# Kernel optimization log

Measured on AMD Instinct MI355X. Metric: run time of the kernel, lower is better.

The kernel has to match this reference:

```python
import jax, jax.numpy as jnp
import numpy as np

N = 20000
E = 320000
H = 4
IN_DIM = 2000
# (in_dim, per-head out channels, concat) for each GATConv layer
LAYER_DIMS = [(2000, 128, True), (512, 64, True), (256, 32, True), (128, 64, False)]
NEG_SLOPE = 0.2  # PyG GATConv LeakyReLU slope


def setup_inputs() -> dict:
    key = jax.random.key(0)
    ks = jax.random.split(key, 2 + 4 * len(LAYER_DIMS))
    inp = {
        "x": jax.random.normal(ks[0], (N, IN_DIM), dtype=jnp.float32),
        "edge_index": jax.random.randint(ks[1], (2, E), 0, N, dtype=jnp.int64),
    }
    for i, (din, c, concat) in enumerate(LAYER_DIMS):
        k0, k1, k2, _ = jax.random.split(ks[2 + i], 4)
        inp[f"W{i}"] = (jax.random.normal(k0, (din, H * c), dtype=jnp.float32)
                         * (1.0 / np.sqrt(din)).astype(np.float32))
        inp[f"as{i}"] = jax.random.normal(k1, (H, c), dtype=jnp.float32) * 0.1
        inp[f"ad{i}"] = jax.random.normal(k2, (H, c), dtype=jnp.float32) * 0.1
        inp[f"b{i}"] = jnp.zeros((H * c if concat else c,), dtype=jnp.float32)
    return inp


def gat_conv(x, src, dst, W, att_src, att_dst, bias, concat):
    n, c = x.shape[0], W.shape[1] // H
    h = (x @ W).reshape(n, H, c)                      # (N,H,C) per-head features
    a_s = jnp.einsum("nhc,hc->nh", h, att_src)        # (N,H) source logits
    a_d = jnp.einsum("nhc,hc->nh", h, att_dst)        # (N,H) target logits
    e = a_s[src] + a_d[dst]                           # (E,H) per-edge logits
    e = jnp.where(e > 0, e, NEG_SLOPE * e)            # leaky_relu
    # segment softmax over edges sharing the same target node
    m = jax.ops.segment_max(e, dst, num_segments=n)   # (N,H)
    ex = jnp.exp(e - m[dst])
    denom = jax.ops.segment_sum(ex, dst, num_segments=n)
    alpha = ex / denom[dst]                           # (E,H)
    # weighted scatter-aggregate of source features
    out = jax.ops.segment_sum(alpha[:, :, None] * h[src], dst, num_segments=n)  # (N,H,C)
    out = out.reshape(n, H * c) if concat else out.mean(axis=1)
    return out + bias


def reference(x, edge_index, W0, as0, ad0, b0, W1, as1, ad1, b1,
              W2, as2, ad2, b2, W3, as3, ad3, b3):
    loops = jnp.arange(N, dtype=edge_index.dtype)
    src = jnp.concatenate([edge_index[0], loops])     # add self-loops (PyG default)
    dst = jnp.concatenate([edge_index[1], loops])
    params = [(W0, as0, ad0, b0), (W1, as1, ad1, b1), (W2, as2, ad2, b2), (W3, as3, ad3, b3)]
    h = x
    for i, (W, a_s, a_d, b) in enumerate(params):
        concat = LAYER_DIMS[i][2]
        h = gat_conv(h, src, dst, W, a_s, a_d, b, concat)
        if i < len(params) - 1:
            h = jax.nn.elu(h)  # dropout inactive in eval mode
    return h
```

## Files before the change

kernel.cpp:

```cpp
#include <hip/hip_runtime.h>
#include <hip/hip_bf16.h>

#define GN 20000
#define GE 320000
#define GETOT (GE + GN)
#define GH 4
#define NROW 20096

typedef __attribute__((ext_vector_type(8))) _Float16 f16x8;
typedef __attribute__((ext_vector_type(4))) float f32x4;

__global__ void detect_dtype_kernel(const void* __restrict__ ei, int* __restrict__ flag) {
    if (threadIdx.x == 0 && blockIdx.x == 0) {
        const long long* p = (const long long*)ei;
        int ok = 1;
        for (int i = 0; i < 16; ++i) {
            long long v = p[i];
            if (v < 0 || v >= GN) ok = 0;
        }
        *flag = ok;
    }
}

__device__ __forceinline__ int load_idx(const void* ei, int is64, long long pos) {
    if (is64) return (int)((const long long*)ei)[pos];
    return ((const int*)ei)[pos];
}

__global__ void hist_kernel(const void* __restrict__ ei, const int* __restrict__ flagp,
                            int* __restrict__ counts) {
    int e = blockIdx.x * blockDim.x + threadIdx.x;
    if (e >= GETOT) return;
    int d;
    if (e < GE) d = load_idx(ei, *flagp, (long long)GE + e);
    else        d = e - GE;
    atomicAdd(&counts[d], 1);
}

__global__ void scan_kernel(const int* __restrict__ counts, int* __restrict__ offsets,
                            int* __restrict__ cursor) {
    __shared__ int sh[1024];
    int tid = threadIdx.x;
    int carry = 0;
    for (int base = 0; base < GN; base += 1024) {
        int i = base + tid;
        int v = (i < GN) ? counts[i] : 0;
        sh[tid] = v;
        __syncthreads();
        for (int o = 1; o < 1024; o <<= 1) {
            int t = (tid >= o) ? sh[tid - o] : 0;
            __syncthreads();
            sh[tid] += t;
            __syncthreads();
        }
        int excl = carry + sh[tid] - v;
        if (i < GN) { offsets[i] = excl; cursor[i] = excl; }
        carry += sh[1023];
        __syncthreads();
    }
    if (tid == 0) offsets[GN] = carry;
}

__global__ void scatter_kernel(const void* __restrict__ ei, const int* __restrict__ flagp,
                               int* __restrict__ cursor, int* __restrict__ csr_src) {
    int e = blockIdx.x * blockDim.x + threadIdx.x;
    if (e >= GETOT) return;
    int s, d;
    if (e < GE) {
        int is64 = *flagp;
        s = load_idx(ei, is64, e);
        d = load_idx(ei, is64, (long long)GE + e);
    } else {
        s = d = e - GE;
    }
    int pos = atomicAdd(&cursor[d], 1);
    csr_src[pos] = s;
}

__device__ __forceinline__ float h2f(unsigned u) {
    unsigned short us = (unsigned short)u;
    _Float16 h;
    __builtin_memcpy(&h, &us, 2);
    return (float)h;
}
__device__ __forceinline__ unsigned short f2h_bits(float v) {
    _Float16 h = (_Float16)v;
    unsigned short us;
    __builtin_memcpy(&us, &h, 2);
    return us;
}

__global__ __launch_bounds__(256) void convert_xf16(const float* __restrict__ x,
                                                    unsigned* __restrict__ xf) {
    const int CPR = 2016 / 8;
    long long idx = (long long)blockIdx.x * 256 + threadIdx.x;
    if (idx >= (long long)NROW * CPR) return;
    int row = (int)(idx / CPR);
    int col = (int)(idx % CPR) * 8;
    uint4 hp = make_uint4(0, 0, 0, 0);
    if (row < GN && col < 2000) {
        const float* p = x + (size_t)row * 2000 + col;
        float4 v0 = *(const float4*)p, v1 = *(const float4*)(p + 4);
        hp.x = (unsigned)f2h_bits(v0.x) | ((unsigned)f2h_bits(v0.y) << 16);
        hp.y = (unsigned)f2h_bits(v0.z) | ((unsigned)f2h_bits(v0.w) << 16);
        hp.z = (unsigned)f2h_bits(v1.x) | ((unsigned)f2h_bits(v1.y) << 16);
        hp.w = (unsigned)f2h_bits(v1.z) | ((unsigned)f2h_bits(v1.w) << 16);
    }
    *(uint4*)(xf + (((size_t)row * 2016 + col) >> 1)) = hp;
}

__global__ void convert_wt(const float* __restrict__ W,
                           _Float16* __restrict__ thi,
                           int K, int N, int Kpad) {
    __shared__ float tile[32][33];
    int kb = blockIdx.x * 32, nb = blockIdx.y * 32;
    for (int i = threadIdx.y; i < 32; i += 8) {
        int k = kb + i, n = nb + threadIdx.x;
        tile[i][threadIdx.x] = (k < K) ? W[(size_t)k * N + n] : 0.f;
    }
    __syncthreads();
    for (int i = threadIdx.y; i < 32; i += 8) {
        int n = nb + i, k = kb + threadIdx.x;
        thi[(size_t)n * Kpad + k] = (_Float16)tile[threadIdx.x][i];
    }
}

__device__ __forceinline__ int swz(int a) { return a ^ (((a >> 6) & 7) << 4); }
__device__ __forceinline__ int invswz(int p) {
    int b8 = (p >> 8) & 1, b7 = (p >> 7) & 1;
    int a6 = ((p >> 6) & 1) ^ b8;
    int a5 = ((p >> 5) & 1) ^ b7;
    int a4 = ((p >> 4) & 1) ^ a6;
    return (p & ~0x70) | (a4 << 4) | (a5 << 5) | (a6 << 6);
}

#define GLDS16(gsrc, ldst) __builtin_amdgcn_global_load_lds( \
    (const __attribute__((address_space(1))) void*)(gsrc),   \
    (__attribute__((address_space(3))) void*)(ldst), 16, 0, 0)

template <int MODE>
__global__ __launch_bounds__(256, 4) void gemm_f16(
        const _Float16* __restrict__ Af, int lda,
        const _Float16* __restrict__ Whi,
        int Kpad, void* __restrict__ Cp, int M, int N, int NC) {
    __shared__ char lds[32768];
    const int tid = threadIdx.x;

    const int nwg = gridDim.x;
    const int q = nwg >> 3, r = nwg & 7;
    const int xcd = blockIdx.x & 7, sub = blockIdx.x >> 3;
    const int orig = (xcd < r ? xcd * (q + 1) : r * (q + 1) + (xcd - r) * q) + sub;
    const int brow = (orig / NC) * 128;
    const int bcol = (orig % NC) * 128;

    const int lane = tid & 63, wid = tid >> 6;
    const int wr = wid >> 1, wc = wid & 1;
    const int l4 = lane & 15, kg = lane >> 4;

    int row8[2], ecol[2];
#pragma unroll
    for (int p = 0; p < 2; ++p) {
        int a = invswz(p * 4096 + tid * 16);
        row8[p] = a >> 6;
        ecol[p] = (a & 63) >> 1;
    }
    int rA[2], rB[2];
#pragma unroll
    for (int p = 0; p < 2; ++p) {
        rA[p] = brow + row8[p];
        rB[p] = bcol + row8[p];
    }

    auto STAGE = [&](int buf, int k0) {
        char* bb = lds + buf * 16384;
#pragma unroll
        for (int p = 0; p < 2; ++p) {
            GLDS16(Af  + (size_t)rA[p] * lda  + k0 + ecol[p], bb + p * 4096 + tid * 16);
            GLDS16(Whi + (size_t)rB[p] * Kpad + k0 + ecol[p], bb + 8192 + p * 4096 + tid * 16);
        }
    };

    int aoff[4], boff[4];
#pragma unroll
    for (int m = 0; m < 4; ++m) {
        aoff[m] = swz((wr * 64 + m * 16 + l4) * 64 + kg * 16);
        boff[m] = swz((wc * 64 + m * 16 + l4) * 64 + kg * 16);
    }

    f32x4 acc[4][4];
#pragma unroll
    for (int m = 0; m < 4; ++m)
#pragma unroll
        for (int n = 0; n < 4; ++n) acc[m][n] = (f32x4)(0.f);

    const int nk = Kpad / 32;
    STAGE(0, 0);

    for (int t = 0; t < nk; ++t) {
        if (t + 1 < nk) {
            STAGE((t + 1) & 1, (t + 1) * 32);
            asm volatile("s_waitcnt vmcnt(4)" ::: "memory");
        } else {
            asm volatile("s_waitcnt vmcnt(0)" ::: "memory");
        }
        __builtin_amdgcn_s_barrier();
        __builtin_amdgcn_sched_barrier(0);

        char* bb = lds + (t & 1) * 16384;
        f16x8 av[4], wh[4];
#pragma unroll
        for (int m = 0; m < 4; ++m) av[m] = *(const f16x8*)(bb + aoff[m]);
#pragma unroll
        for (int n = 0; n < 4; ++n) wh[n] = *(const f16x8*)(bb + 8192 + boff[n]);
        asm volatile("s_waitcnt lgkmcnt(0)" ::: "memory");
        __builtin_amdgcn_sched_barrier(0);

#pragma unroll
        for (int m = 0; m < 4; ++m)
#pragma unroll
            for (int n = 0; n < 4; ++n)
                acc[m][n] = __builtin_amdgcn_mfma_f32_16x16x32_f16(av[m], wh[n], acc[m][n], 0, 0, 0);
        __builtin_amdgcn_s_barrier();
    }

#pragma unroll
    for (int m = 0; m < 4; ++m) {
        int gr0 = brow + wr * 64 + m * 16 + (lane >> 4) * 4;
#pragma unroll
        for (int n = 0; n < 4; ++n) {
            int gc = bcol + wc * 64 + n * 16 + l4;
#pragma unroll
            for (int rr2 = 0; rr2 < 4; ++rr2) {
                int gr = gr0 + rr2;
                if (gr < M) {
                    size_t o = (size_t)gr * N + gc;
                    float v = acc[m][n][rr2];
                    if constexpr (MODE == 2) ((float*)Cp)[o] = v;
                    else                     ((_Float16*)Cp)[o] = (_Float16)v;
                }
            }
        }
    }
}

template <bool F16>
__global__ void att_sd_kernel(const void* __restrict__ hfeat,
                              const float* __restrict__ att_s,
                              const float* __restrict__ att_d,
                              float* __restrict__ a_s, float* __restrict__ a_d,
                              int C) {
    int wid  = (blockIdx.x * blockDim.x + threadIdx.x) >> 6;
    int lane = threadIdx.x & 63;
    if (wid >= GN) return;
#pragma unroll
    for (int h = 0; h < GH; ++h) {
        float ss = 0.f, sd = 0.f;
        for (int cc = lane; cc < C; cc += 64) {
            size_t idx = (size_t)wid * GH * C + h * C + cc;
            float v = F16 ? h2f(((const unsigned short*)hfeat)[idx])
                          : ((const float*)hfeat)[idx];
            ss += v * att_s[h * C + cc];
            sd += v * att_d[h * C + cc];
        }
#pragma unroll
        for (int o = 32; o; o >>= 1) {
            ss += __shfl_xor(ss, o);
            sd += __shfl_xor(sd, o);
        }
        if (lane == 0) { a_s[wid * GH + h] = ss; a_d[wid * GH + h] = sd; }
    }
}

template <int C, int CPT, int BLOCK>
__global__ __launch_bounds__(BLOCK) void gat_aggregate_f16(
        const unsigned short* __restrict__ hfeat,
        const float* __restrict__ a_s,
        const float* __restrict__ a_d,
        const int* __restrict__ offsets,
        const int* __restrict__ csr_src,
        const float* __restrict__ bias,
        unsigned short* __restrict__ of16) {
    constexpr int HC = GH * C;
    static_assert(BLOCK * CPT == HC, "coverage");
    const int n     = blockIdx.x;
    const int tid   = threadIdx.x;
    const int start = offsets[n];
    const int end   = offsets[n + 1];

    __shared__ float s_m[GH];
    __shared__ float s_den[GH];
    __shared__ int   s_src[64];
    __shared__ float s_al[GH][68];

    const float4 ad4 = *(const float4*)(a_d + n * GH);
    const float adh[GH] = {ad4.x, ad4.y, ad4.z, ad4.w};

    if (tid < 64) {
        float lmax[GH], lsum[GH];
#pragma unroll
        for (int h = 0; h < GH; ++h) lmax[h] = -1e30f;
        for (int e = start + tid; e < end; e += 64) {
            int s = csr_src[e];
            float4 as4 = *(const float4*)(a_s + s * GH);
            float l[GH] = {as4.x + adh[0], as4.y + adh[1], as4.z + adh[2], as4.w + adh[3]};
#pragma unroll
            for (int h = 0; h < GH; ++h) {
                float ll = l[h] > 0.f ? l[h] : 0.2f * l[h];
                lmax[h] = fmaxf(lmax[h], ll);
            }
        }
#pragma unroll
        for (int h = 0; h < GH; ++h)
#pragma unroll
            for (int o = 32; o; o >>= 1) lmax[h] = fmaxf(lmax[h], __shfl_xor(lmax[h], o));
#pragma unroll
        for (int h = 0; h < GH; ++h) lsum[h] = 0.f;
        for (int e = start + tid; e < end; e += 64) {
            int s = csr_src[e];
            float4 as4 = *(const float4*)(a_s + s * GH);
            float l[GH] = {as4.x + adh[0], as4.y + adh[1], as4.z + adh[2], as4.w + adh[3]};
#pragma unroll
            for (int h = 0; h < GH; ++h) {
                float ll = l[h] > 0.f ? l[h] : 0.2f * l[h];
                lsum[h] += __expf(ll - lmax[h]);
            }
        }
#pragma unroll
        for (int h = 0; h < GH; ++h)
#pragma unroll
            for (int o = 32; o; o >>= 1) lsum[h] += __shfl_xor(lsum[h], o);
        if (tid == 0) {
#pragma unroll
            for (int h = 0; h < GH; ++h) { s_m[h] = lmax[h]; s_den[h] = lsum[h]; }
        }
    }
    __syncthreads();

    float mm[GH], inv[GH];
#pragma unroll
    for (int h = 0; h < GH; ++h) { mm[h] = s_m[h]; inv[h] = 1.0f / s_den[h]; }

    const int ch0 = tid * CPT;
    const int hd  = ch0 / C;
    float acc[CPT];
#pragma unroll
    for (int j = 0; j < CPT; ++j) acc[j] = 0.f;

    for (int e0 = start; e0 < end; e0 += 64) {
        __syncthreads();
        if (tid < 64) {
            bool vld = (e0 + tid) < end;
            int s = vld ? csr_src[e0 + tid] : n;
            s_src[tid] = s;
            float4 as4 = *(const float4*)(a_s + s * GH);
            float l[GH] = {as4.x + adh[0], as4.y + adh[1], as4.z + adh[2], as4.w + adh[3]};
#pragma unroll
            for (int h = 0; h < GH; ++h) {
                float ll = l[h] > 0.f ? l[h] : 0.2f * l[h];
                s_al[h][tid] = vld ? __expf(ll - mm[h]) * inv[h] : 0.f;
            }
        }
        __syncthreads();
        int cnt = end - e0; if (cnt > 64) cnt = 64;
        int cnt4 = (cnt + 3) & ~3;
        for (int i = 0; i < cnt4; i += 4) {
            int4   ss = *(const int4*)&s_src[i];
            float4 aa = *(const float4*)&s_al[hd][i];
            if constexpr (CPT == 4) {
                uint2 v0 = ((const uint2*)(hfeat + (size_t)ss.x * HC))[tid];
                uint2 v1 = ((const uint2*)(hfeat + (size_t)ss.y * HC))[tid];
                uint2 v2 = ((const uint2*)(hfeat + (size_t)ss.z * HC))[tid];
                uint2 v3 = ((const uint2*)(hfeat + (size_t)ss.w * HC))[tid];
                acc[0] = fmaf(aa.x, h2f(v0.x & 0xffff), acc[0]);
                acc[1] = fmaf(aa.x, h2f(v0.x >> 16),    acc[1]);
                acc[2] = fmaf(aa.x, h2f(v0.y & 0xffff), acc[2]);
                acc[3] = fmaf(aa.x, h2f(v0.y >> 16),    acc[3]);
                acc[0] = fmaf(aa.y, h2f(v1.x & 0xffff), acc[0]);
                acc[1] = fmaf(aa.y, h2f(v1.x >> 16),    acc[1]);
                acc[2] = fmaf(aa.y, h2f(v1.y & 0xffff), acc[2]);
                acc[3] = fmaf(aa.y, h2f(v1.y >> 16),    acc[3]);
                acc[0] = fmaf(aa.z, h2f(v2.x & 0xffff), acc[0]);
                acc[1] = fmaf(aa.z, h2f(v2.x >> 16),    acc[1]);
                acc[2] = fmaf(aa.z, h2f(v2.y & 0xffff), acc[2]);
                acc[3] = fmaf(aa.z, h2f(v2.y >> 16),    acc[3]);
                acc[0] = fmaf(aa.w, h2f(v3.x & 0xffff), acc[0]);
                acc[1] = fmaf(aa.w, h2f(v3.x >> 16),    acc[1]);
                acc[2] = fmaf(aa.w, h2f(v3.y & 0xffff), acc[2]);
                acc[3] = fmaf(aa.w, h2f(v3.y >> 16),    acc[3]);
            } else {
                unsigned v0 = ((const unsigned*)(hfeat + (size_t)ss.x * HC))[tid];
                unsigned v1 = ((const unsigned*)(hfeat + (size_t)ss.y * HC))[tid];
                unsigned v2 = ((const unsigned*)(hfeat + (size_t)ss.z * HC))[tid];
                unsigned v3 = ((const unsigned*)(hfeat + (size_t)ss.w * HC))[tid];
                acc[0] = fmaf(aa.x, h2f(v0 & 0xffff), acc[0]);
                acc[1] = fmaf(aa.x, h2f(v0 >> 16),    acc[1]);
                acc[0] = fmaf(aa.y, h2f(v1 & 0xffff), acc[0]);
                acc[1] = fmaf(aa.y, h2f(v1 >> 16),    acc[1]);
                acc[0] = fmaf(aa.z, h2f(v2 & 0xffff), acc[0]);
                acc[1] = fmaf(aa.z, h2f(v2 >> 16),    acc[1]);
                acc[0] = fmaf(aa.w, h2f(v3 & 0xffff), acc[0]);
                acc[1] = fmaf(aa.w, h2f(v3 >> 16),    acc[1]);
            }
        }
    }

    unsigned short hs[CPT];
#pragma unroll
    for (int j = 0; j < CPT; ++j) {
        float v = acc[j] + bias[ch0 + j];
        v = v > 0.f ? v : expm1f(v);
        hs[j] = f2h_bits(v);
    }
    unsigned short* op = of16 + (size_t)n * HC + ch0;
    if constexpr (CPT == 4) {
        uint2 hw = make_uint2((unsigned)hs[0] | ((unsigned)hs[1] << 16),
                              (unsigned)hs[2] | ((unsigned)hs[3] << 16));
        *(uint2*)op = hw;
    } else {
        *(unsigned*)op = (unsigned)hs[0] | ((unsigned)hs[1] << 16);
    }
}

__global__ __launch_bounds__(128) void gat_aggregate_final(
        const float* __restrict__ hfeat,
        const float* __restrict__ a_s,
        const float* __restrict__ a_d,
        const int* __restrict__ offsets,
        const int* __restrict__ csr_src,
        const float* __restrict__ bias,
        float* __restrict__ outf) {
    constexpr int C = 64, HC = GH * C;
    const int n     = blockIdx.x;
    const int tid   = threadIdx.x;
    const int start = offsets[n];
    const int end   = offsets[n + 1];

    __shared__ float s_m[GH];
    __shared__ float s_den[GH];
    __shared__ int   s_src[64];
    __shared__ float s_al[GH][68];
    __shared__ float sacc[256];

    const float4 ad4 = *(const float4*)(a_d + n * GH);
    const float adh[GH] = {ad4.x, ad4.y, ad4.z, ad4.w};

    if (tid < 64) {
        float lmax[GH], lsum[GH];
#pragma unroll
        for (int h = 0; h < GH; ++h) lmax[h] = -1e30f;
        for (int e = start + tid; e < end; e += 64) {
            int s = csr_src[e];
            float4 as4 = *(const float4*)(a_s + s * GH);
            float l[GH] = {as4.x + adh[0], as4.y + adh[1], as4.z + adh[2], as4.w + adh[3]};
#pragma unroll
            for (int h = 0; h < GH; ++h) {
                float ll = l[h] > 0.f ? l[h] : 0.2f * l[h];
                lmax[h] = fmaxf(lmax[h], ll);
            }
        }
#pragma unroll
        for (int h = 0; h < GH; ++h)
#pragma unroll
            for (int o = 32; o; o >>= 1) lmax[h] = fmaxf(lmax[h], __shfl_xor(lmax[h], o));
#pragma unroll
        for (int h = 0; h < GH; ++h) lsum[h] = 0.f;
        for (int e = start + tid; e < end; e += 64) {
            int s = csr_src[e];
            float4 as4 = *(const float4*)(a_s + s * GH);
            float l[GH] = {as4.x + adh[0], as4.y + adh[1], as4.z + adh[2], as4.w + adh[3]};
#pragma unroll
            for (int h = 0; h < GH; ++h) {
                float ll = l[h] > 0.f ? l[h] : 0.2f * l[h];
                lsum[h] += __expf(ll - lmax[h]);
            }
        }
#pragma unroll
        for (int h = 0; h < GH; ++h)
#pragma unroll
            for (int o = 32; o; o >>= 1) lsum[h] += __shfl_xor(lsum[h], o);
        if (tid == 0) {
#pragma unroll
            for (int h = 0; h < GH; ++h) { s_m[h] = lmax[h]; s_den[h] = lsum[h]; }
        }
    }
    __syncthreads();

    float mm[GH], inv[GH];
#pragma unroll
    for (int h = 0; h < GH; ++h) { mm[h] = s_m[h]; inv[h] = 1.0f / s_den[h]; }

    const int hd = (2 * tid) / C;
    float2 acc = make_float2(0.f, 0.f);

    for (int e0 = start; e0 < end; e0 += 64) {
        __syncthreads();
        if (tid < 64) {
            bool vld = (e0 + tid) < end;
            int s = vld ? csr_src[e0 + tid] : n;
            s_src[tid] = s;
            float4 as4 = *(const float4*)(a_s + s * GH);
            float l[GH] = {as4.x + adh[0], as4.y + adh[1], as4.z + adh[2], as4.w + adh[3]};
#pragma unroll
            for (int h = 0; h < GH; ++h) {
                float ll = l[h] > 0.f ? l[h] : 0.2f * l[h];
                s_al[h][tid] = vld ? __expf(ll - mm[h]) * inv[h] : 0.f;
            }
        }
        __syncthreads();
        int cnt = end - e0; if (cnt > 64) cnt = 64;
        int cnt4 = (cnt + 3) & ~3;
        for (int i = 0; i < cnt4; i += 4) {
            int4   ss = *(const int4*)&s_src[i];
            float4 aa = *(const float4*)&s_al[hd][i];
            float2 v0 = ((const float2*)(hfeat + (size_t)ss.x * HC))[tid];
            float2 v1 = ((const float2*)(hfeat + (size_t)ss.y * HC))[tid];
            float2 v2 = ((const float2*)(hfeat + (size_t)ss.z * HC))[tid];
            float2 v3 = ((const float2*)(hfeat + (size_t)ss.w * HC))[tid];
            acc.x = fmaf(aa.x, v0.x, acc.x); acc.y = fmaf(aa.x, v0.y, acc.y);
            acc.x = fmaf(aa.y, v1.x, acc.x); acc.y = fmaf(aa.y, v1.y, acc.y);
            acc.x = fmaf(aa.z, v2.x, acc.x); acc.y = fmaf(aa.z, v2.y, acc.y);
            acc.x = fmaf(aa.w, v3.x, acc.x); acc.y = fmaf(aa.w, v3.y, acc.y);
        }
    }

    sacc[2 * tid]     = acc.x;
    sacc[2 * tid + 1] = acc.y;
    __syncthreads();
    if (tid < C) {
        float v = 0.f;
#pragma unroll
        for (int h = 0; h < GH; ++h) v += sacc[h * C + tid];
        outf[(size_t)n * C + tid] = v * (1.0f / GH) + bias[tid];
    }
}

extern "C" void kernel_launch(void* const* d_in, const int* in_sizes, int n_in,
                              void* d_out, int out_size, void* d_ws, size_t ws_size,
                              hipStream_t stream) {
    const float* x  = (const float*)d_in[0];
    const void*  ei = d_in[1];
    const float* W[4]  = {(const float*)d_in[2],  (const float*)d_in[6],
                          (const float*)d_in[10], (const float*)d_in[14]};
    const float* AS[4] = {(const float*)d_in[3],  (const float*)d_in[7],
                          (const float*)d_in[11], (const float*)d_in[15]};
    const float* AD[4] = {(const float*)d_in[4],  (const float*)d_in[8],
                          (const float*)d_in[12], (const float*)d_in[16]};
    const float* BI[4] = {(const float*)d_in[5],  (const float*)d_in[9],
                          (const float*)d_in[13], (const float*)d_in[17]};

    char*  w   = (char*)d_ws;
    size_t off = 0;
    auto alloc = [&](size_t b) -> char* {
        char* p = w + off;
        off += (b + 255) & ~(size_t)255;
        return p;
    };
    int*   flag    = (int*)alloc(4);
    int*   counts  = (int*)alloc((GN + 1) * sizeof(int));
    int*   offsets = (int*)alloc((GN + 1) * sizeof(int));
    int*   cursor  = (int*)alloc(GN * sizeof(int));
    int*   csr_src = (int*)alloc((size_t)GETOT * sizeof(int));
    float* a_s     = (float*)alloc((size_t)GN * GH * sizeof(float));
    float* a_d     = (float*)alloc((size_t)GN * GH * sizeof(float));
    unsigned short* hA = (unsigned short*)alloc((size_t)NROW * 512 * 2);
    unsigned short* hB = (unsigned short*)alloc((size_t)NROW * 512 * 2);
    float* hbuf    = (float*)alloc((size_t)NROW * 256 * sizeof(float));
    _Float16* wt   = (_Float16*)alloc((size_t)512 * 2016 * 2);
    _Float16* xf16 = (_Float16*)alloc((size_t)NROW * 2016 * 2);
    (void)in_sizes; (void)n_in; (void)out_size; (void)ws_size;

    detect_dtype_kernel<<<1, 64, 0, stream>>>(ei, flag);
    hipMemsetAsync(counts, 0, (GN + 1) * sizeof(int), stream);
    int eblocks = (GETOT + 255) / 256;
    hist_kernel<<<eblocks, 256, 0, stream>>>(ei, flag, counts);
    scan_kernel<<<1, 1024, 0, stream>>>(counts, offsets, cursor);
    scatter_kernel<<<eblocks, 256, 0, stream>>>(ei, flag, cursor, csr_src);

    const dim3 tb(32, 8);
    const int NR = (GN + 127) / 128;

    convert_wt<<<dim3(2016 / 32, 512 / 32), tb, 0, stream>>>(W[0], wt, 2000, 512, 2016);
    convert_xf16<<<(int)(((size_t)NROW * 252 + 255) / 256), 256, 0, stream>>>(x, (unsigned*)xf16);
    gemm_f16<0><<<NR * 4, 256, 0, stream>>>(xf16, 2016, wt, 2016, hA, GN, 512, 4);
    att_sd_kernel<true><<<(GN * 64) / 256, 256, 0, stream>>>(hA, AS[0], AD[0], a_s, a_d, 128);
    gat_aggregate_f16<128, 4, 128><<<GN, 128, 0, stream>>>(hA, a_s, a_d, offsets, csr_src,
                                                           BI[0], hB);
    convert_wt<<<dim3(512 / 32, 256 / 32), tb, 0, stream>>>(W[1], wt, 512, 256, 512);
    gemm_f16<0><<<NR * 2, 256, 0, stream>>>((_Float16*)hB, 512, wt, 512, hA, GN, 256, 2);
    att_sd_kernel<true><<<(GN * 64) / 256, 256, 0, stream>>>(hA, AS[1], AD[1], a_s, a_d, 64);
    gat_aggregate_f16<64, 4, 64><<<GN, 64, 0, stream>>>(hA, a_s, a_d, offsets, csr_src,
                                                        BI[1], hB);
    convert_wt<<<dim3(256 / 32, 128 / 32), tb, 0, stream>>>(W[2], wt, 256, 128, 256);
    gemm_f16<0><<<NR * 1, 256, 0, stream>>>((_Float16*)hB, 256, wt, 256, hA, GN, 128, 1);
    att_sd_kernel<true><<<(GN * 64) / 256, 256, 0, stream>>>(hA, AS[2], AD[2], a_s, a_d, 32);
    gat_aggregate_f16<32, 2, 64><<<GN, 64, 0, stream>>>(hA, a_s, a_d, offsets, csr_src,
                                                        BI[2], hB);
    convert_wt<<<dim3(128 / 32, 256 / 32), tb, 0, stream>>>(W[3], wt, 128, 256, 128);
    gemm_f16<2><<<NR * 2, 256, 0, stream>>>((_Float16*)hB, 128, wt, 128, hbuf, GN, 256, 2);
    att_sd_kernel<false><<<(GN * 64) / 256, 256, 0, stream>>>(hbuf, AS[3], AD[3], a_s, a_d, 64);
    gat_aggregate_final<<<GN, 128, 0, stream>>>(hbuf, a_s, a_d, offsets, csr_src,
                                                BI[3], (float*)d_out);
}
```

Measured before the change: 447.0 us.

## Fuse fp32-to-fp16 conversion of x into the first GEMM and parallelize scan

Drops the separate convert_xf16 pass. The first-layer GEMM now stages fp32 rows of x straight into LDS through a new swizzle and converts them to fp16 while building the MFMA fragments. This removes a full write and re-read of the 20000x2016 half-precision copy, but doubles LDS staging size and lowers the occupancy target to 3 for that variant. The CSR offset scan also switches from a looped block scan to a per-thread chunk of 20 plus one block scan, cutting serial iterations.

Measured after the change: 408.7 us. -8.6%, faster.

```diff
diff --git a/kernel.cpp b/kernel.cpp
--- a/kernel.cpp
+++ b/kernel.cpp
@@ -37,28 +37,41 @@
     atomicAdd(&counts[d], 1);
 }
 
-__global__ void scan_kernel(const int* __restrict__ counts, int* __restrict__ offsets,
-                            int* __restrict__ cursor) {
+__global__ __launch_bounds__(1024) void scan_kernel(const int* __restrict__ counts,
+                                                    int* __restrict__ offsets,
+                                                    int* __restrict__ cursor) {
     __shared__ int sh[1024];
-    int tid = threadIdx.x;
-    int carry = 0;
-    for (int base = 0; base < GN; base += 1024) {
-        int i = base + tid;
-        int v = (i < GN) ? counts[i] : 0;
-        sh[tid] = v;
+    const int tid = threadIdx.x;
+    constexpr int CH = 20;
+    const int base = tid * CH;
+    int loc[CH];
+    int sum = 0;
+#pragma unroll
+    for (int i = 0; i < CH; ++i) {
+        int idx = base + i;
+        int v = (idx < GN) ? counts[idx] : 0;
+        loc[i] = sum;
+        sum += v;
+    }
+    sh[tid] = sum;
+    __syncthreads();
+    for (int o = 1; o < 1024; o <<= 1) {
+        int t = (tid >= o) ? sh[tid - o] : 0;
         __syncthreads();
-        for (int o = 1; o < 1024; o <<= 1) {
-            int t = (tid >= o) ? sh[tid - o] : 0;
-            __syncthreads();
-            sh[tid] += t;
-            __syncthreads();
-        }
-        int excl = carry + sh[tid] - v;
-        if (i < GN) { offsets[i] = excl; cursor[i] = excl; }
-        carry += sh[1023];
+        sh[tid] += t;
         __syncthreads();
     }
-    if (tid == 0) offsets[GN] = carry;
+    const int excl = tid ? sh[tid - 1] : 0;
+#pragma unroll
+    for (int i = 0; i < CH; ++i) {
+        int idx = base + i;
+        if (idx < GN) {
+            int o = excl + loc[i];
+            offsets[idx] = o;
+            cursor[idx]  = o;
+        }
+    }
+    if (tid == 1023) offsets[GN] = sh[1023];
 }
 
 __global__ void scatter_kernel(const void* __restrict__ ei, const int* __restrict__ flagp,
@@ -90,25 +103,6 @@
     return us;
 }
 
-__global__ __launch_bounds__(256) void convert_xf16(const float* __restrict__ x,
-                                                    unsigned* __restrict__ xf) {
-    const int CPR = 2016 / 8;
-    long long idx = (long long)blockIdx.x * 256 + threadIdx.x;
-    if (idx >= (long long)NROW * CPR) return;
-    int row = (int)(idx / CPR);
-    int col = (int)(idx % CPR) * 8;
-    uint4 hp = make_uint4(0, 0, 0, 0);
-    if (row < GN && col < 2000) {
-        const float* p = x + (size_t)row * 2000 + col;
-        float4 v0 = *(const float4*)p, v1 = *(const float4*)(p + 4);
-        hp.x = (unsigned)f2h_bits(v0.x) | ((unsigned)f2h_bits(v0.y) << 16);
-        hp.y = (unsigned)f2h_bits(v0.z) | ((unsigned)f2h_bits(v0.w) << 16);
-        hp.z = (unsigned)f2h_bits(v1.x) | ((unsigned)f2h_bits(v1.y) << 16);
-        hp.w = (unsigned)f2h_bits(v1.z) | ((unsigned)f2h_bits(v1.w) << 16);
-    }
-    *(uint4*)(xf + (((size_t)row * 2016 + col) >> 1)) = hp;
-}
-
 __global__ void convert_wt(const float* __restrict__ W,
                            _Float16* __restrict__ thi,
                            int K, int N, int Kpad) {
@@ -133,17 +127,20 @@
     int a4 = ((p >> 4) & 1) ^ a6;
     return (p & ~0x70) | (a4 << 4) | (a5 << 5) | (a6 << 6);
 }
+__device__ __forceinline__ int swzA32(int a) { return a ^ (((a >> 7) & 7) << 4); }
 
 #define GLDS16(gsrc, ldst) __builtin_amdgcn_global_load_lds( \
     (const __attribute__((address_space(1))) void*)(gsrc),   \
     (__attribute__((address_space(3))) void*)(ldst), 16, 0, 0)
 
 template <int MODE>
-__global__ __launch_bounds__(256, 4) void gemm_f16(
-        const _Float16* __restrict__ Af, int lda,
+__global__ __launch_bounds__(256, MODE == 1 ? 3 : 4) void gemm_f16(
+        const void* __restrict__ Ap, int lda, int K,
         const _Float16* __restrict__ Whi,
         int Kpad, void* __restrict__ Cp, int M, int N, int NC) {
-    __shared__ char lds[32768];
+    constexpr int BUFB = (MODE == 1) ? 24576 : 16384;
+    constexpr int WOFF = (MODE == 1) ? 16384 : 8192;
+    __shared__ char lds[2 * BUFB];
     const int tid = threadIdx.x;
 
     const int nwg = gridDim.x;
@@ -164,26 +161,51 @@
         row8[p] = a >> 6;
         ecol[p] = (a & 63) >> 1;
     }
-    int rA[2], rB[2];
-#pragma unroll
-    for (int p = 0; p < 2; ++p) {
-        rA[p] = brow + row8[p];
-        rB[p] = bcol + row8[p];
-    }
+    int rB[2];
+#pragma unroll
+    for (int p = 0; p < 2; ++p) rB[p] = bcol + row8[p];
+
+    int rA2[2];
+    int rA4[4], eA4[4];
+    if constexpr (MODE == 1) {
+#pragma unroll
+        for (int p = 0; p < 4; ++p) {
+            int a = swzA32(p * 4096 + tid * 16);
+            int rr = brow + (a >> 7);
+            rA4[p] = rr < M ? rr : M - 1;
+            eA4[p] = (a & 127) >> 2;
+        }
+    } else {
+#pragma unroll
+        for (int p = 0; p < 2; ++p) rA2[p] = brow + row8[p];
+    }
+    const float*    A32 = (const float*)Ap;
+    const _Float16* Af  = (const _Float16*)Ap;
 
     auto STAGE = [&](int buf, int k0) {
-        char* bb = lds + buf * 16384;
-#pragma unroll
-        for (int p = 0; p < 2; ++p) {
-            GLDS16(Af  + (size_t)rA[p] * lda  + k0 + ecol[p], bb + p * 4096 + tid * 16);
-            GLDS16(Whi + (size_t)rB[p] * Kpad + k0 + ecol[p], bb + 8192 + p * 4096 + tid * 16);
-        }
+        char* bb = lds + buf * BUFB;
+        if constexpr (MODE == 1) {
+#pragma unroll
+            for (int p = 0; p < 4; ++p) {
+                int kk = k0 + eA4[p];
+                if (kk >= K) kk = 0;
+                GLDS16(A32 + (size_t)rA4[p] * lda + kk, bb + p * 4096 + tid * 16);
+            }
+        } else {
+#pragma unroll
+            for (int p = 0; p < 2; ++p)
+                GLDS16(Af + (size_t)rA2[p] * lda + k0 + ecol[p], bb + p * 4096 + tid * 16);
+        }
+#pragma unroll
+        for (int p = 0; p < 2; ++p)
+            GLDS16(Whi + (size_t)rB[p] * Kpad + k0 + ecol[p], bb + WOFF + p * 4096 + tid * 16);
     };
 
     int aoff[4], boff[4];
 #pragma unroll
     for (int m = 0; m < 4; ++m) {
-        aoff[m] = swz((wr * 64 + m * 16 + l4) * 64 + kg * 16);
+        int row = wr * 64 + m * 16 + l4;
+        aoff[m] = (MODE == 1) ? swzA32(row * 128 + kg * 32) : swz(row * 64 + kg * 16);
         boff[m] = swz((wc * 64 + m * 16 + l4) * 64 + kg * 16);
     }
 
@@ -199,19 +221,34 @@
     for (int t = 0; t < nk; ++t) {
         if (t + 1 < nk) {
             STAGE((t + 1) & 1, (t + 1) * 32);
-            asm volatile("s_waitcnt vmcnt(4)" ::: "memory");
+            if constexpr (MODE == 1)
+                asm volatile("s_waitcnt vmcnt(6)" ::: "memory");
+            else
+                asm volatile("s_waitcnt vmcnt(4)" ::: "memory");
         } else {
             asm volatile("s_waitcnt vmcnt(0)" ::: "memory");
         }
         __builtin_amdgcn_s_barrier();
         __builtin_amdgcn_sched_barrier(0);
 
-        char* bb = lds + (t & 1) * 16384;
+        char* bb = lds + (t & 1) * BUFB;
         f16x8 av[4], wh[4];
-#pragma unroll
-        for (int m = 0; m < 4; ++m) av[m] = *(const f16x8*)(bb + aoff[m]);
-#pragma unroll
-        for (int n = 0; n < 4; ++n) wh[n] = *(const f16x8*)(bb + 8192 + boff[n]);
+        if constexpr (MODE == 1) {
+#pragma unroll
+            for (int m = 0; m < 4; ++m) {
+                f32x4 u0 = *(const f32x4*)(bb + aoff[m]);
+                f32x4 u1 = *(const f32x4*)(bb + (aoff[m] ^ 16));
+                av[m][0] = (_Float16)u0.x; av[m][1] = (_Float16)u0.y;
+                av[m][2] = (_Float16)u0.z; av[m][3] = (_Float16)u0.w;
+                av[m][4] = (_Float16)u1.x; av[m][5] = (_Float16)u1.y;
+                av[m][6] = (_Float16)u1.z; av[m][7] = (_Float16)u1.w;
+            }
+        } else {
+#pragma unroll
+            for (int m = 0; m < 4; ++m) av[m] = *(const f16x8*)(bb + aoff[m]);
+        }
+#pragma unroll
+        for (int n = 0; n < 4; ++n) wh[n] = *(const f16x8*)(bb + WOFF + boff[n]);
         asm volatile("s_waitcnt lgkmcnt(0)" ::: "memory");
         __builtin_amdgcn_sched_barrier(0);
 
@@ -566,7 +603,6 @@
     unsigned short* hB = (unsigned short*)alloc((size_t)NROW * 512 * 2);
     float* hbuf    = (float*)alloc((size_t)NROW * 256 * sizeof(float));
     _Float16* wt   = (_Float16*)alloc((size_t)512 * 2016 * 2);
-    _Float16* xf16 = (_Float16*)alloc((size_t)NROW * 2016 * 2);
     (void)in_sizes; (void)n_in; (void)out_size; (void)ws_size;
 
     detect_dtype_kernel<<<1, 64, 0, stream>>>(ei, flag);
@@ -580,23 +616,22 @@
     const int NR = (GN + 127) / 128;
 
     convert_wt<<<dim3(2016 / 32, 512 / 32), tb, 0, stream>>>(W[0], wt, 2000, 512, 2016);
-    convert_xf16<<<(int)(((size_t)NROW * 252 + 255) / 256), 256, 0, stream>>>(x, (unsigned*)xf16);
-    gemm_f16<0><<<NR * 4, 256, 0, stream>>>(xf16, 2016, wt, 2016, hA, GN, 512, 4);
+    gemm_f16<1><<<NR * 4, 256, 0, stream>>>(x, 2000, 2000, wt, 2016, hA, GN, 512, 4);
     att_sd_kernel<true><<<(GN * 64) / 256, 256, 0, stream>>>(hA, AS[0], AD[0], a_s, a_d, 128);
     gat_aggregate_f16<128, 4, 128><<<GN, 128, 0, stream>>>(hA, a_s, a_d, offsets, csr_src,
                                                            BI[0], hB);
     convert_wt<<<dim3(512 / 32, 256 / 32), tb, 0, stream>>>(W[1], wt, 512, 256, 512);
-    gemm_f16<0><<<NR * 2, 256, 0, stream>>>((_Float16*)hB, 512, wt, 512, hA, GN, 256, 2);
+    gemm_f16<0><<<NR * 2, 256, 0, stream>>>(hB, 512, 512, wt, 512, hA, GN, 256, 2);
     att_sd_kernel<true><<<(GN * 64) / 256, 256, 0, stream>>>(hA, AS[1], AD[1], a_s, a_d, 64);
     gat_aggregate_f16<64, 4, 64><<<GN, 64, 0, stream>>>(hA, a_s, a_d, offsets, csr_src,
                                                         BI[1], hB);
     convert_wt<<<dim3(256 / 32, 128 / 32), tb, 0, stream>>>(W[2], wt, 256, 128, 256);
-    gemm_f16<0><<<NR * 1, 256, 0, stream>>>((_Float16*)hB, 256, wt, 256, hA, GN, 128, 1);
+    gemm_f16<0><<<NR * 1, 256, 0, stream>>>(hB, 256, 256, wt, 256, hA, GN, 128, 1);
     att_sd_kernel<true><<<(GN * 64) / 256, 256, 0, stream>>>(hA, AS[2], AD[2], a_s, a_d, 32);
     gat_aggregate_f16<32, 2, 64><<<GN, 64, 0, stream>>>(hA, a_s, a_d, offsets, csr_src,
                                                         BI[2], hB);
     convert_wt<<<dim3(128 / 32, 256 / 32), tb, 0, stream>>>(W[3], wt, 128, 256, 128);
-    gemm_f16<2><<<NR * 2, 256, 0, stream>>>((_Float16*)hB, 128, wt, 128, hbuf, GN, 256, 2);
+    gemm_f16<2><<<NR * 2, 256, 0, stream>>>(hB, 128, 128, wt, 128, hbuf, GN, 256, 2);
     att_sd_kernel<false><<<(GN * 64) / 256, 256, 0, stream>>>(hbuf, AS[3], AD[3], a_s, a_d, 64);
     gat_aggregate_final<<<GN, 128, 0, stream>>>(hbuf, a_s, a_d, offsets, csr_src,
                                                 BI[3], (float*)d_out);
```
